# Optimization experiments

Hardware: AMD Instinct MI355X
Metric: run time of the kernel (lower is better)

Reference implementation:

```python
import jax, jax.numpy as jnp
import numpy as np

N = 100000
IN_CH = 128
OUT_CH = 128
E = 1600000


def setup_inputs() -> dict:
    key = jax.random.key(0)
    k1, k2, k3, k4 = jax.random.split(key, 4)
    x = jax.random.normal(k1, (N, IN_CH), dtype=jnp.float32)
    edge_index = jax.random.randint(k2, (2, E), 0, N, dtype=jnp.int64)
    # Glorot-style init for the GCNConv linear weight, zero bias (PyG default)
    W = jax.random.normal(k3, (IN_CH, OUT_CH), dtype=jnp.float32) * (1.0 / np.sqrt(IN_CH))
    b = jnp.zeros((OUT_CH,), dtype=jnp.float32)
    return {"x": x, "edge_index": edge_index, "W": W, "b": b}


def reference(x, edge_index, W, b):
    n = x.shape[0]
    # ---- add self loops (PyG GCNConv default add_self_loops=True) ----
    loops = jnp.arange(n, dtype=edge_index.dtype)
    row = jnp.concatenate([edge_index[0], loops])  # source
    col = jnp.concatenate([edge_index[1], loops])  # target
    # ---- symmetric degree normalization: D^{-1/2} (A+I) D^{-1/2} ----
    ones = jnp.ones(col.shape[0], dtype=x.dtype)
    deg = jax.ops.segment_sum(ones, col, num_segments=n)  # in-degree incl. self loop
    deg_inv_sqrt = jnp.where(deg > 0, jax.lax.rsqrt(deg), 0.0)
    norm = deg_inv_sqrt[row] * deg_inv_sqrt[col]  # [E+N]
    # ---- linear transform then gather-scale-scatter aggregation ----
    h = x @ W  # [N, OUT_CH]
    msgs = norm[:, None] * h[row]  # [E+N, OUT_CH]
    out = jax.ops.segment_sum(msgs, col, num_segments=n) + b  # [N, OUT_CH]
    # ---- ReLU ----
    return jax.nn.relu(out)
```

## Files before the change

kernel.cpp:

```cpp
#include <hip/hip_runtime.h>
#include <hip/hip_bf16.h>
#include <hip/hip_fp16.h>

#define IN_CH 128
#define OUT_CH 128
#define TM 64
#define TMF 128
#define CHUNK 8192
#define NPB 512
#define BSHIFT 9
#define CPAD 16
#define CAPT 16384

typedef __attribute__((ext_vector_type(8))) short short8;
typedef __attribute__((ext_vector_type(4))) float f32x4;

__device__ __forceinline__ unsigned short f2bf(float f) {
    union { float f; unsigned u; } v; v.f = f;
    unsigned r = v.u + 0x7FFFu + ((v.u >> 16) & 1u);
    return (unsigned short)(r >> 16);
}


__global__ __launch_bounds__(256) void init_kernel(int* __restrict__ cursor,
                                                   const float* __restrict__ W,
                                                   unsigned short* __restrict__ Wf,
                                                   int NBK) {
    int t = threadIdx.x;
    if (blockIdx.x == 0) {
        if (t < NBK) cursor[t * CPAD] = t * CAPT;
        return;
    }
    int base = (blockIdx.x - 1) * 2048;
#pragma unroll
    for (int rep = 0; rep < 8; ++rep) {
        int idx = base + rep * 256 + t;
        int j = idx & 7;
        int lane = (idx >> 3) & 63;
        int ctks = idx >> 9;
        int ks = ctks & 3;
        int ct = ctks >> 2;
        int k = ks * 32 + (lane >> 4) * 8 + j;
        int nc = ct * 16 + (lane & 15);
        Wf[idx] = f2bf(W[k * 128 + nc]);
    }
}

__global__ __launch_bounds__(512) void part_gemm_kernel(const int* __restrict__ row,
                                                        const int* __restrict__ col,
                                                        int* __restrict__ cursor,
                                                        int* __restrict__ tmp,
                                                        const float* __restrict__ A,
                                                        const unsigned short* __restrict__ Wf,
                                                        __half* __restrict__ G,
                                                        int E, int n, int NBK, int vec,
                                                        int nchunks) {
    __shared__ int lcnt[256];
    __shared__ int lstart[256];
    __shared__ int lbase[256];
    __shared__ int lscan[256];
    __shared__ int buf[CHUNK];
    __shared__ unsigned char bid[CHUNK];
    int t = threadIdx.x;
    if (blockIdx.x >= nchunks) {
        int gb = blockIdx.x - nchunks;
        int w = t >> 6;
        int lane = t & 63;
        int m = lane & 15;
        int quad = lane >> 4;
        int rowi = gb * TMF + w * 16 + m;
        short8 af[4];
        if (rowi < n) {
            const f32x4* Ar = (const f32x4*)(A + (size_t)rowi * 128);
#pragma unroll
            for (int ks = 0; ks < 4; ++ks) {
                f32x4 v0 = __builtin_nontemporal_load(Ar + ks * 8 + quad * 2);
                f32x4 v1 = __builtin_nontemporal_load(Ar + ks * 8 + quad * 2 + 1);
                short8 a;
                a[0] = (short)f2bf(v0.x); a[1] = (short)f2bf(v0.y);
                a[2] = (short)f2bf(v0.z); a[3] = (short)f2bf(v0.w);
                a[4] = (short)f2bf(v1.x); a[5] = (short)f2bf(v1.y);
                a[6] = (short)f2bf(v1.z); a[7] = (short)f2bf(v1.w);
                af[ks] = a;
            }
        } else {
#pragma unroll
            for (int ks = 0; ks < 4; ++ks) af[ks] = (short8)0;
        }
        int grow_base = gb * TMF + w * 16 + quad * 4;
        const short8* B8 = (const short8*)Wf;
#pragma unroll
        for (int ct = 0; ct < 8; ++ct) {
            f32x4 acc = {0.f, 0.f, 0.f, 0.f};
#pragma unroll
            for (int ks = 0; ks < 4; ++ks) {
                short8 bf = B8[(ct * 4 + ks) * 64 + lane];
                acc = __builtin_amdgcn_mfma_f32_16x16x32_bf16(af[ks], bf, acc, 0, 0, 0);
            }
            int nc = ct * 16 + m;
#pragma unroll
            for (int reg = 0; reg < 4; ++reg) {
                int grow = grow_base + reg;
                if (grow < n)
                    G[(size_t)grow * 128 + nc] = __float2half(acc[reg]);
            }
        }
        return;
    }
    int base = blockIdx.x * CHUNK;
    int nloc = min(CHUNK, E - base);
    if (t < 256) lcnt[t] = 0;
    __syncthreads();
    if (vec) {
        const int4* c4 = (const int4*)(col + base);
        int nv = nloc >> 2;
        for (int i = t; i < nv; i += 512) {
            int4 c = c4[i];
            atomicAdd(&lcnt[c.x >> BSHIFT], 1);
            atomicAdd(&lcnt[c.y >> BSHIFT], 1);
            atomicAdd(&lcnt[c.z >> BSHIFT], 1);
            atomicAdd(&lcnt[c.w >> BSHIFT], 1);
        }
        for (int i = (nv << 2) + t; i < nloc; i += 512)
            atomicAdd(&lcnt[col[base + i] >> BSHIFT], 1);
    } else {
        for (int i = t; i < nloc; i += 512)
            atomicAdd(&lcnt[col[base + i] >> BSHIFT], 1);
    }
    __syncthreads();
    int v = 0;
    if (t < 256) { v = lcnt[t]; lscan[t] = v; }
    __syncthreads();
    for (int off = 1; off < 256; off <<= 1) {
        int a = 0, b2 = 0;
        if (t < 256) { a = lscan[t]; b2 = (t >= off) ? lscan[t - off] : 0; }
        __syncthreads();
        if (t < 256) lscan[t] = a + b2;
        __syncthreads();
    }
    if (t < 256) {
        int excl = lscan[t] - v;
        lstart[t] = excl;
        lcnt[t] = excl;
        lbase[t] = (t < NBK && v) ? atomicAdd(&cursor[t * CPAD], v) : 0;
    }
    __syncthreads();
    if (vec) {
        const int4* c4 = (const int4*)(col + base);
        const int4* r4 = (const int4*)(row + base);
        int nv = nloc >> 2;
        for (int i = t; i < nv; i += 512) {
            int4 c = c4[i];
            int4 r = r4[i];
            int b0 = c.x >> BSHIFT, p0 = atomicAdd(&lcnt[b0], 1);
            buf[p0] = r.x | ((c.x & (NPB - 1)) << 20); bid[p0] = (unsigned char)b0;
            int b1 = c.y >> BSHIFT, p1 = atomicAdd(&lcnt[b1], 1);
            buf[p1] = r.y | ((c.y & (NPB - 1)) << 20); bid[p1] = (unsigned char)b1;
            int b2 = c.z >> BSHIFT, p2 = atomicAdd(&lcnt[b2], 1);
            buf[p2] = r.z | ((c.z & (NPB - 1)) << 20); bid[p2] = (unsigned char)b2;
            int b3 = c.w >> BSHIFT, p3 = atomicAdd(&lcnt[b3], 1);
            buf[p3] = r.w | ((c.w & (NPB - 1)) << 20); bid[p3] = (unsigned char)b3;
        }
        for (int i = (nv << 2) + t; i < nloc; i += 512) {
            int c = col[base + i], r = row[base + i];
            int b = c >> BSHIFT, p = atomicAdd(&lcnt[b], 1);
            buf[p] = r | ((c & (NPB - 1)) << 20); bid[p] = (unsigned char)b;
        }
    } else {
        for (int i = t; i < nloc; i += 512) {
            int c = col[base + i], r = row[base + i];
            int b = c >> BSHIFT, p = atomicAdd(&lcnt[b], 1);
            buf[p] = r | ((c & (NPB - 1)) << 20); bid[p] = (unsigned char)b;
        }
    }
    __syncthreads();
    for (int i = t; i < nloc; i += 512) {
        int b = bid[i];
        int gidx = lbase[b] + (i - lstart[b]);
        if (gidx < (b + 1) * CAPT) tmp[gidx] = buf[i];
    }
}

__global__ __launch_bounds__(512) void csr_build_kernel(const int* __restrict__ tmp,
                                                        const int* __restrict__ cursor,
                                                        int* __restrict__ offs,
                                                        float* __restrict__ dis,
                                                        int* __restrict__ srcs,
                                                        int N, int NBK) {
    __shared__ int cnt[NPB];
    __shared__ int cur[NPB];
    __shared__ int bsum[256];
    int b = blockIdx.x;
    int t = threadIdx.x;
    cnt[t] = 0;
    if (t < 256) bsum[t] = (t < NBK) ? min(cursor[t * CPAD] - t * CAPT, CAPT) : 0;
    __syncthreads();
    for (int off = 1; off < 256; off <<= 1) {
        int a = 0, b2 = 0;
        if (t < 256) { a = bsum[t]; b2 = (t >= off) ? bsum[t - off] : 0; }
        __syncthreads();
        if (t < 256) bsum[t] = a + b2;
        __syncthreads();
    }
    int wbeg = b * CAPT;
    int cnt_b = min(cursor[b * CPAD] - wbeg, CAPT);
    int cbeg = bsum[b] - cnt_b;
    if (b == 0 && t == 0) offs[N] = bsum[NBK - 1];
    for (int e = t; e < cnt_b; e += 512)
        atomicAdd(&cnt[(tmp[wbeg + e] >> 20)], 1);
    __syncthreads();
    int v0 = 0, v1 = 0, s = 0;
    if (t < 256) { v0 = cnt[2 * t]; v1 = cnt[2 * t + 1]; s = v0 + v1; cur[t] = s; }
    __syncthreads();
    for (int off = 1; off < 256; off <<= 1) {
        int a = 0, b2 = 0;
        if (t < 256) { a = cur[t]; b2 = (t >= off) ? cur[t - off] : 0; }
        __syncthreads();
        if (t < 256) cur[t] = a + b2;
        __syncthreads();
    }
    int excl_pair = 0;
    if (t < 256) excl_pair = cur[t] - s;
    __syncthreads();
    if (t < 256) {
        int e0 = excl_pair;
        int e1 = excl_pair + v0;
        cur[2 * t] = e0;
        cur[2 * t + 1] = e1;
        int n0 = b * NPB + 2 * t;
        int n1 = n0 + 1;
        if (n0 < N) { offs[n0] = cbeg + e0; dis[n0] = rsqrtf((float)(v0 + 1)); }
        if (n1 < N) { offs[n1] = cbeg + e1; dis[n1] = rsqrtf((float)(v1 + 1)); }
    }
    __syncthreads();
    for (int e = t; e < cnt_b; e += 512) {
        int p = tmp[wbeg + e];
        int slot = atomicAdd(&cur[p >> 20], 1);
        srcs[cbeg + slot] = p & 0xFFFFF;
    }
}

__global__ __launch_bounds__(256) void aggregate_g16_kernel(
        const __half2* __restrict__ g2, const int* __restrict__ srcs,
        const int* __restrict__ offs, const float* __restrict__ dis,
        const float* __restrict__ bias, float2* __restrict__ out2, int n) {
    int gid = blockIdx.x * blockDim.x + threadIdx.x;
    int wid = gid >> 6;
    int lane = gid & 63;
    if (wid >= n) return;
    int widu = __builtin_amdgcn_readfirstlane(wid);
    int beg = offs[widu];
    int end = offs[widu + 1];
    float di = dis[widu];
    float2 xi = __half22float2(g2[((size_t)widu << 6) + lane]);
    float accx = di * xi.x;
    float accy = di * xi.y;
    int e = beg;
    for (; e + 8 <= end; e += 8) {
        int s0 = __builtin_amdgcn_readfirstlane(srcs[e]);
        int s1 = __builtin_amdgcn_readfirstlane(srcs[e + 1]);
        int s2 = __builtin_amdgcn_readfirstlane(srcs[e + 2]);
        int s3 = __builtin_amdgcn_readfirstlane(srcs[e + 3]);
        int s4 = __builtin_amdgcn_readfirstlane(srcs[e + 4]);
        int s5 = __builtin_amdgcn_readfirstlane(srcs[e + 5]);
        int s6 = __builtin_amdgcn_readfirstlane(srcs[e + 6]);
        int s7 = __builtin_amdgcn_readfirstlane(srcs[e + 7]);
        float d0 = dis[s0], d1 = dis[s1], d2 = dis[s2], d3 = dis[s3];
        float d4 = dis[s4], d5 = dis[s5], d6 = dis[s6], d7 = dis[s7];
        float2 v0 = __half22float2(g2[((size_t)s0 << 6) + lane]);
        float2 v1 = __half22float2(g2[((size_t)s1 << 6) + lane]);
        float2 v2 = __half22float2(g2[((size_t)s2 << 6) + lane]);
        float2 v3 = __half22float2(g2[((size_t)s3 << 6) + lane]);
        float2 v4 = __half22float2(g2[((size_t)s4 << 6) + lane]);
        float2 v5 = __half22float2(g2[((size_t)s5 << 6) + lane]);
        float2 v6 = __half22float2(g2[((size_t)s6 << 6) + lane]);
        float2 v7 = __half22float2(g2[((size_t)s7 << 6) + lane]);
        float tx0 = fmaf(d0, v0.x, d1 * v1.x);
        float tx1 = fmaf(d2, v2.x, d3 * v3.x);
        float tx2 = fmaf(d4, v4.x, d5 * v5.x);
        float tx3 = fmaf(d6, v6.x, d7 * v7.x);
        accx += (tx0 + tx1) + (tx2 + tx3);
        float ty0 = fmaf(d0, v0.y, d1 * v1.y);
        float ty1 = fmaf(d2, v2.y, d3 * v3.y);
        float ty2 = fmaf(d4, v4.y, d5 * v5.y);
        float ty3 = fmaf(d6, v6.y, d7 * v7.y);
        accy += (ty0 + ty1) + (ty2 + ty3);
    }
    for (; e + 4 <= end; e += 4) {
        int s0 = __builtin_amdgcn_readfirstlane(srcs[e]);
        int s1 = __builtin_amdgcn_readfirstlane(srcs[e + 1]);
        int s2 = __builtin_amdgcn_readfirstlane(srcs[e + 2]);
        int s3 = __builtin_amdgcn_readfirstlane(srcs[e + 3]);
        float d0 = dis[s0], d1 = dis[s1], d2 = dis[s2], d3 = dis[s3];
        float2 v0 = __half22float2(g2[((size_t)s0 << 6) + lane]);
        float2 v1 = __half22float2(g2[((size_t)s1 << 6) + lane]);
        float2 v2 = __half22float2(g2[((size_t)s2 << 6) + lane]);
        float2 v3 = __half22float2(g2[((size_t)s3 << 6) + lane]);
        accx += fmaf(d0, v0.x, d1 * v1.x) + fmaf(d2, v2.x, d3 * v3.x);
        accy += fmaf(d0, v0.y, d1 * v1.y) + fmaf(d2, v2.y, d3 * v3.y);
    }
    for (; e < end; ++e) {
        int s = __builtin_amdgcn_readfirstlane(srcs[e]);
        float ds = dis[s];
        float2 v = __half22float2(g2[((size_t)s << 6) + lane]);
        accx = fmaf(ds, v.x, accx);
        accy = fmaf(ds, v.y, accy);
    }
    float2 bv = ((const float2*)bias)[lane];
    float2 r;
    r.x = fmaxf(fmaf(di, accx, bv.x), 0.f);
    r.y = fmaxf(fmaf(di, accy, bv.y), 0.f);
    out2[((size_t)widu << 6) + lane] = r;
}

__global__ __launch_bounds__(256) void gemm_g16_kernel(const float* __restrict__ A,
        const float* __restrict__ W, __half* __restrict__ G, int n) {
    __shared__ __half Wh[128 * 128];
    __shared__ float As[TM * 128];
    int t = threadIdx.x;
    const float4* W4 = (const float4*)W;
#pragma unroll
    for (int j = 0; j < 16; ++j) {
        int idx = t + 256 * j;
        float4 v = W4[idx];
        __half2 p0 = __floats2half2_rn(v.x, v.y);
        __half2 p1 = __floats2half2_rn(v.z, v.w);
        *(__half2*)&Wh[idx * 4]     = p0;
        *(__half2*)&Wh[idx * 4 + 2] = p1;
    }
    int row0 = blockIdx.x * TM;
    const float4* A4 = (const float4*)A;
#pragma unroll
    for (int j = 0; j < 8; ++j) {
        int idx = t + 256 * j;
        int r = idx >> 5;
        int c4 = idx & 31;
        int gr = row0 + r;
        float4 v = make_float4(0.f, 0.f, 0.f, 0.f);
        if (gr < n) v = A4[(size_t)gr * 32 + c4];
        *(float4*)&As[r * 128 + c4 * 4] = v;
    }
    __syncthreads();
    int tcol = t & 15;
    int trow = t >> 4;
    int cb = tcol * 8;
    float acc[4][8];
#pragma unroll
    for (int r = 0; r < 4; ++r)
#pragma unroll
        for (int c = 0; c < 8; ++c) acc[r][c] = 0.f;
    const float* Abase = &As[(trow * 4) * 128];
#pragma unroll 4
    for (int k = 0; k < 128; ++k) {
        float4 wv = *(const float4*)&Wh[k * 128 + cb];
        const __half2* wh = (const __half2*)&wv;
        float2 w01 = __half22float2(wh[0]);
        float2 w23 = __half22float2(wh[1]);
        float2 w45 = __half22float2(wh[2]);
        float2 w67 = __half22float2(wh[3]);
        float wreg[8] = {w01.x, w01.y, w23.x, w23.y, w45.x, w45.y, w67.x, w67.y};
#pragma unroll
        for (int r = 0; r < 4; ++r) {
            float a = Abase[r * 128 + k];
#pragma unroll
            for (int c = 0; c < 8; ++c) acc[r][c] = fmaf(a, wreg[c], acc[r][c]);
        }
    }
#pragma unroll
    for (int r = 0; r < 4; ++r) {
        int gr = row0 + trow * 4 + r;
        if (gr < n) {
            __half2 o[4];
#pragma unroll
            for (int j = 0; j < 4; ++j)
                o[j] = __floats2half2_rn(acc[r][2 * j], acc[r][2 * j + 1]);
            *(float4*)&G[(size_t)gr * 128 + cb] = *(float4*)o;
        }
    }
}

__global__ void count_kernel(const int* __restrict__ col, int* __restrict__ deg, int E) {
    int i = blockIdx.x * blockDim.x + threadIdx.x;
    if (i < E) atomicAdd(&deg[col[i]], 1);
}

__global__ void scan_block_kernel(const int* __restrict__ in, int* __restrict__ out,
                                  int* __restrict__ bsums, float* __restrict__ dis, int n) {
    __shared__ int lds[256];
    int t = threadIdx.x;
    int base = blockIdx.x * 1024;
    int v[4];
    int idx = base + t * 4;
#pragma unroll
    for (int j = 0; j < 4; ++j) v[j] = (idx + j < n) ? in[idx + j] : 0;
#pragma unroll
    for (int j = 0; j < 4; ++j)
        if (idx + j < n) dis[idx + j] = rsqrtf((float)(v[j] + 1));
    int sum = v[0] + v[1] + v[2] + v[3];
    lds[t] = sum;
    __syncthreads();
    for (int off = 1; off < 256; off <<= 1) {
        int a = lds[t];
        int bq = (t >= off) ? lds[t - off] : 0;
        __syncthreads();
        lds[t] = a + bq;
        __syncthreads();
    }
    int run = (t == 0) ? 0 : lds[t - 1];
    if (t == 255 && bsums) bsums[blockIdx.x] = lds[255];
#pragma unroll
    for (int j = 0; j < 4; ++j) {
        if (idx + j < n) out[idx + j] = run;
        run += v[j];
    }
}

__global__ void scan_sums_kernel(int* __restrict__ bsums, int nB) {
    __shared__ int lds[256];
    int t = threadIdx.x;
    lds[t] = (t < nB) ? bsums[t] : 0;
    __syncthreads();
    for (int off = 1; off < 256; off <<= 1) {
        int a = lds[t];
        int bq = (t >= off) ? lds[t - off] : 0;
        __syncthreads();
        lds[t] = a + bq;
        __syncthreads();
    }
    if (t < nB) bsums[t] = (t == 0) ? 0 : lds[t - 1];
}

__global__ void scan_add_kernel(int* __restrict__ offs, const int* __restrict__ bsums,
                                int n, int total) {
    int i = blockIdx.x * blockDim.x + threadIdx.x;
    if (i < n) offs[i] += bsums[i >> 10];
    if (i == 0) offs[n] = total;
}

__global__ void fill_kernel(const int* __restrict__ row, const int* __restrict__ col,
                            const int* __restrict__ offs, int* __restrict__ deg,
                            int* __restrict__ srcs, int E) {
    int i = blockIdx.x * blockDim.x + threadIdx.x;
    if (i < E) {
        int c = col[i];
        int old = atomicSub(&deg[c], 1);
        srcs[offs[c] + old - 1] = row[i];
    }
}

__global__ __launch_bounds__(256) void aggregate_f32_kernel(
        const float2* __restrict__ x2, const int* __restrict__ srcs,
        const int* __restrict__ offs, const float* __restrict__ dis,
        float2* __restrict__ out2, int n) {
    int gid = blockIdx.x * blockDim.x + threadIdx.x;
    int wid = gid >> 6;
    int lane = gid & 63;
    if (wid >= n) return;
    int beg = offs[wid];
    int end = offs[wid + 1];
    float di = dis[wid];
    float2 xi = x2[(size_t)wid * 64 + lane];
    float accx = di * xi.x;
    float accy = di * xi.y;
    for (int e = beg; e < end; ++e) {
        int s = srcs[e];
        float ds = dis[s];
        float2 xs = x2[(size_t)s * 64 + lane];
        accx = fmaf(ds, xs.x, accx);
        accy = fmaf(ds, xs.y, accy);
    }
    float2 r;
    r.x = di * accx;
    r.y = di * accy;
    out2[(size_t)wid * 64 + lane] = r;
}

__global__ __launch_bounds__(256) void gemm_inplace_kernel(float* __restrict__ io,
                                                           const float* __restrict__ W,
                                                           const float* __restrict__ bias, int n) {
    __shared__ float rowL[128];
    __shared__ float part[128];
    int t = threadIdx.x;
    int c = t & 127;
    int half = t >> 7;
    float w[64];
#pragma unroll
    for (int j = 0; j < 64; ++j) w[j] = W[(half * 64 + j) * 128 + c];
    float bv = bias[c];
    int kbase = half * 64;
    for (int r = blockIdx.x; r < n; r += gridDim.x) {
        if (t < 128) rowL[t] = io[(size_t)r * 128 + t];
        __syncthreads();
        float acc = 0.f;
#pragma unroll
        for (int j = 0; j < 64; ++j) acc = fmaf(rowL[kbase + j], w[j], acc);
        if (half) part[c] = acc;
        __syncthreads();
        if (!half) {
            float v = acc + part[c] + bv;
            io[(size_t)r * 128 + c] = fmaxf(v, 0.f);
        }
        __syncthreads();
    }
}

extern "C" void kernel_launch(void* const* d_in, const int* in_sizes, int n_in,
                              void* d_out, int out_size, void* d_ws, size_t ws_size,
                              hipStream_t stream) {
    const float* x  = (const float*)d_in[0];
    const int*   ei = (const int*)d_in[1];
    const float* W  = (const float*)d_in[2];
    const float* b  = (const float*)d_in[3];
    float* out = (float*)d_out;

    int N = in_sizes[0] / IN_CH;
    int E = in_sizes[1] / 2;
    const int* rowp = ei;
    const int* colp = ei + E;
    int NBK = (N + NPB - 1) >> BSHIFT;
    int tpb = 256;
    int nchunks = (E + CHUNK - 1) / CHUNK;
    int gemmBlocks = (N + TMF - 1) / TMF;

    char* p = (char*)d_ws;
    auto take = [&](size_t bytes) { char* q = p; p += (bytes + 255) & ~(size_t)255; return q; };
    int*    cursor = (int*)take((size_t)256 * CPAD * 4);
    int*    offs   = (int*)take((size_t)(N + 1) * 4);
    float*  dis    = (float*)take((size_t)N * 4);
    int*    srcs   = (int*)take((size_t)E * 4);
    __half* g      = (__half*)take((size_t)N * 128 * 2);
    unsigned short* Wf = (unsigned short*)take((size_t)16384 * 2);
    bool fast = (NBK <= 256) && ((size_t)(p - (char*)d_ws) <= ws_size) &&
                ((size_t)NBK * CAPT <= (size_t)out_size) && (N < (1 << 20)) &&
                ((size_t)E + NPB <= (size_t)CAPT * NBK);

    long long threads_agg = (long long)N * 64;
    int agg_blocks = (int)((threads_agg + tpb - 1) / tpb);

    if (fast) {
        int* tmp = (int*)d_out;
        int vec = (((uintptr_t)colp | (uintptr_t)rowp) & 15) == 0 ? 1 : 0;
        init_kernel<<<9, 256, 0, stream>>>(cursor, W, Wf, NBK);
        part_gemm_kernel<<<nchunks + gemmBlocks, 512, 0, stream>>>(
            rowp, colp, cursor, tmp, x, Wf, g, E, N, NBK, vec, nchunks);
        csr_build_kernel<<<NBK, 512, 0, stream>>>(tmp, cursor, offs, dis, srcs, N, NBK);
        aggregate_g16_kernel<<<agg_blocks, tpb, 0, stream>>>(
            (const __half2*)g, srcs, offs, dis, b, (float2*)out, N);
    } else {
        char* q = (char*)d_ws;
        auto take2 = [&](size_t bytes) { char* r = q; q += (bytes + 255) & ~(size_t)255; return r; };
        int*    deg2   = (int*)take2((size_t)N * 4);
        int*    offs2  = (int*)take2((size_t)(N + 1) * 4);
        int*    bsums2 = (int*)take2(256 * 4);
        int*    srcs2  = (int*)take2((size_t)E * 4);
        float*  dis2   = (float*)take2((size_t)N * 4);
        __half* g2b    = (__half*)take2((size_t)N * 128 * 2);
        bool fits2 = ((size_t)(q - (char*)d_ws)) <= ws_size;
        hipMemsetAsync(deg2, 0, (size_t)N * 4, stream);
        count_kernel<<<(E + tpb - 1) / tpb, tpb, 0, stream>>>(colp, deg2, E);
        int nB = (N + 1023) / 1024;
        scan_block_kernel<<<nB, 256, 0, stream>>>(deg2, offs2, bsums2, dis2, N);
        scan_sums_kernel<<<1, 256, 0, stream>>>(bsums2, nB);
        scan_add_kernel<<<(N + tpb - 1) / tpb, tpb, 0, stream>>>(offs2, bsums2, N, E);
        fill_kernel<<<(E + tpb - 1) / tpb, tpb, 0, stream>>>(rowp, colp, offs2, deg2, srcs2, E);
        if (fits2) {
            gemm_g16_kernel<<<(N + TM - 1) / TM, 256, 0, stream>>>(x, W, g2b, N);
            aggregate_g16_kernel<<<agg_blocks, tpb, 0, stream>>>(
                (const __half2*)g2b, srcs2, offs2, dis2, b, (float2*)out, N);
        } else {
            aggregate_f32_kernel<<<agg_blocks, tpb, 0, stream>>>(
                (const float2*)x, srcs2, offs2, dis2, (float2*)out, N);
            gemm_inplace_kernel<<<2048, 256, 0, stream>>>(out, W, b, N);
        }
    }
}
```

Baseline: 208.3 us.

## Use register-held atomic slots in partitioning, CSR build, and split-wave aggregation

The edge-partition kernel no longer does a separate count pass, shared scan and shared-memory staging buffer. Each thread now keeps its edges and the LDS atomic slot positions in registers and scatters straight to global memory. The CSR build kernel does the same, reusing the atomic ranks from its count pass so it skips a second global read and a second atomic pass. The aggregation kernel assigns two waves per node, each summing half the edge list, and combines them through shared memory to shorten per-node latency chains. The cost is higher register pressure, uncoalesced global scatter writes, and an extra barrier in aggregation.

```diff
diff --git a/kernel.cpp b/kernel.cpp
--- a/kernel.cpp
+++ b/kernel.cpp
@@ -53,14 +53,10 @@
                                                         const float* __restrict__ A,
                                                         const unsigned short* __restrict__ Wf,
                                                         __half* __restrict__ G,
-                                                        int E, int n, int NBK, int vec,
+                                                        int E, int n, int NBK,
                                                         int nchunks) {
     __shared__ int lcnt[256];
-    __shared__ int lstart[256];
     __shared__ int lbase[256];
-    __shared__ int lscan[256];
-    __shared__ int buf[CHUNK];
-    __shared__ unsigned char bid[CHUNK];
     int t = threadIdx.x;
     if (blockIdx.x >= nchunks) {
         int gb = blockIdx.x - nchunks;
@@ -111,73 +107,36 @@
     int nloc = min(CHUNK, E - base);
     if (t < 256) lcnt[t] = 0;
     __syncthreads();
-    if (vec) {
-        const int4* c4 = (const int4*)(col + base);
-        int nv = nloc >> 2;
-        for (int i = t; i < nv; i += 512) {
-            int4 c = c4[i];
-            atomicAdd(&lcnt[c.x >> BSHIFT], 1);
-            atomicAdd(&lcnt[c.y >> BSHIFT], 1);
-            atomicAdd(&lcnt[c.z >> BSHIFT], 1);
-            atomicAdd(&lcnt[c.w >> BSHIFT], 1);
-        }
-        for (int i = (nv << 2) + t; i < nloc; i += 512)
-            atomicAdd(&lcnt[col[base + i] >> BSHIFT], 1);
-    } else {
-        for (int i = t; i < nloc; i += 512)
-            atomicAdd(&lcnt[col[base + i] >> BSHIFT], 1);
-    }
-    __syncthreads();
-    int v = 0;
-    if (t < 256) { v = lcnt[t]; lscan[t] = v; }
-    __syncthreads();
-    for (int off = 1; off < 256; off <<= 1) {
-        int a = 0, b2 = 0;
-        if (t < 256) { a = lscan[t]; b2 = (t >= off) ? lscan[t - off] : 0; }
-        __syncthreads();
-        if (t < 256) lscan[t] = a + b2;
-        __syncthreads();
-    }
+    int myv[16];
+    int mybp[16];
+#pragma unroll
+    for (int it = 0; it < 16; ++it) {
+        int i = t + it * 512;
+        if (i < nloc) {
+            int c = col[base + i];
+            int r = row[base + i];
+            int b = c >> BSHIFT;
+            int p = atomicAdd(&lcnt[b], 1);
+            myv[it] = r | ((c & (NPB - 1)) << 20);
+            mybp[it] = b | (p << 8);
+        } else {
+            mybp[it] = -1;
+        }
+    }
+    __syncthreads();
     if (t < 256) {
-        int excl = lscan[t] - v;
-        lstart[t] = excl;
-        lcnt[t] = excl;
+        int v = lcnt[t];
         lbase[t] = (t < NBK && v) ? atomicAdd(&cursor[t * CPAD], v) : 0;
     }
     __syncthreads();
-    if (vec) {
-        const int4* c4 = (const int4*)(col + base);
-        const int4* r4 = (const int4*)(row + base);
-        int nv = nloc >> 2;
-        for (int i = t; i < nv; i += 512) {
-            int4 c = c4[i];
-            int4 r = r4[i];
-            int b0 = c.x >> BSHIFT, p0 = atomicAdd(&lcnt[b0], 1);
-            buf[p0] = r.x | ((c.x & (NPB - 1)) << 20); bid[p0] = (unsigned char)b0;
-            int b1 = c.y >> BSHIFT, p1 = atomicAdd(&lcnt[b1], 1);
-            buf[p1] = r.y | ((c.y & (NPB - 1)) << 20); bid[p1] = (unsigned char)b1;
-            int b2 = c.z >> BSHIFT, p2 = atomicAdd(&lcnt[b2], 1);
-            buf[p2] = r.z | ((c.z & (NPB - 1)) << 20); bid[p2] = (unsigned char)b2;
-            int b3 = c.w >> BSHIFT, p3 = atomicAdd(&lcnt[b3], 1);
-            buf[p3] = r.w | ((c.w & (NPB - 1)) << 20); bid[p3] = (unsigned char)b3;
-        }
-        for (int i = (nv << 2) + t; i < nloc; i += 512) {
-            int c = col[base + i], r = row[base + i];
-            int b = c >> BSHIFT, p = atomicAdd(&lcnt[b], 1);
-            buf[p] = r | ((c & (NPB - 1)) << 20); bid[p] = (unsigned char)b;
-        }
-    } else {
-        for (int i = t; i < nloc; i += 512) {
-            int c = col[base + i], r = row[base + i];
-            int b = c >> BSHIFT, p = atomicAdd(&lcnt[b], 1);
-            buf[p] = r | ((c & (NPB - 1)) << 20); bid[p] = (unsigned char)b;
-        }
-    }
-    __syncthreads();
-    for (int i = t; i < nloc; i += 512) {
-        int b = bid[i];
-        int gidx = lbase[b] + (i - lstart[b]);
-        if (gidx < (b + 1) * CAPT) tmp[gidx] = buf[i];
+#pragma unroll
+    for (int it = 0; it < 16; ++it) {
+        if (mybp[it] >= 0) {
+            int b = mybp[it] & 255;
+            int p = mybp[it] >> 8;
+            int gidx = lbase[b] + p;
+            if (gidx < (b + 1) * CAPT) tmp[gidx] = myv[it];
+        }
     }
 }
 
@@ -206,8 +165,19 @@
     int cnt_b = min(cursor[b * CPAD] - wbeg, CAPT);
     int cbeg = bsum[b] - cnt_b;
     if (b == 0 && t == 0) offs[N] = bsum[NBK - 1];
-    for (int e = t; e < cnt_b; e += 512)
-        atomicAdd(&cnt[(tmp[wbeg + e] >> 20)], 1);
+    int myv[32];
+    int myp[32];
+#pragma unroll
+    for (int it = 0; it < 32; ++it) {
+        int e = t + it * 512;
+        if (e < cnt_b) {
+            int p = tmp[wbeg + e];
+            myv[it] = p;
+            myp[it] = atomicAdd(&cnt[p >> 20], 1);
+        } else {
+            myv[it] = -1;
+        }
+    }
     __syncthreads();
     int v0 = 0, v1 = 0, s = 0;
     if (t < 256) { v0 = cnt[2 * t]; v1 = cnt[2 * t + 1]; s = v0 + v1; cur[t] = s; }
@@ -233,30 +203,47 @@
         if (n1 < N) { offs[n1] = cbeg + e1; dis[n1] = rsqrtf((float)(v1 + 1)); }
     }
     __syncthreads();
-    for (int e = t; e < cnt_b; e += 512) {
-        int p = tmp[wbeg + e];
-        int slot = atomicAdd(&cur[p >> 20], 1);
-        srcs[cbeg + slot] = p & 0xFFFFF;
-    }
-}
-
-__global__ __launch_bounds__(256) void aggregate_g16_kernel(
+#pragma unroll
+    for (int it = 0; it < 32; ++it) {
+        if (myv[it] >= 0) {
+            int node = myv[it] >> 20;
+            srcs[cbeg + cur[node] + myp[it]] = myv[it] & 0xFFFFF;
+        }
+    }
+}
+
+__global__ __launch_bounds__(512) void aggregate_g16_kernel(
         const __half2* __restrict__ g2, const int* __restrict__ srcs,
         const int* __restrict__ offs, const float* __restrict__ dis,
         const float* __restrict__ bias, float2* __restrict__ out2, int n) {
-    int gid = blockIdx.x * blockDim.x + threadIdx.x;
-    int wid = gid >> 6;
-    int lane = gid & 63;
-    if (wid >= n) return;
-    int widu = __builtin_amdgcn_readfirstlane(wid);
-    int beg = offs[widu];
-    int end = offs[widu + 1];
-    float di = dis[widu];
-    float2 xi = __half22float2(g2[((size_t)widu << 6) + lane]);
-    float accx = di * xi.x;
-    float accy = di * xi.y;
-    int e = beg;
-    for (; e + 8 <= end; e += 8) {
+    __shared__ float2 part[4][64];
+    int t = threadIdx.x;
+    int lane = t & 63;
+    int wv = t >> 6;
+    int nib = wv >> 1;
+    int half = wv & 1;
+    int node = blockIdx.x * 4 + nib;
+    bool active = node < n;
+    int beg = 0, end = 0;
+    float di = 0.f;
+    int widu = 0;
+    if (active) {
+        widu = __builtin_amdgcn_readfirstlane(node);
+        beg = offs[widu];
+        end = offs[widu + 1];
+        di = dis[widu];
+    }
+    int mid = beg + ((end - beg) >> 1);
+    int lo = half ? mid : beg;
+    int hi = half ? end : mid;
+    float accx = 0.f, accy = 0.f;
+    if (!half && active) {
+        float2 xi = __half22float2(g2[((size_t)widu << 6) + lane]);
+        accx = di * xi.x;
+        accy = di * xi.y;
+    }
+    int e = lo;
+    for (; e + 8 <= hi; e += 8) {
         int s0 = __builtin_amdgcn_readfirstlane(srcs[e]);
         int s1 = __builtin_amdgcn_readfirstlane(srcs[e + 1]);
         int s2 = __builtin_amdgcn_readfirstlane(srcs[e + 2]);
@@ -286,7 +273,7 @@
         float ty3 = fmaf(d6, v6.y, d7 * v7.y);
         accy += (ty0 + ty1) + (ty2 + ty3);
     }
-    for (; e + 4 <= end; e += 4) {
+    for (; e + 4 <= hi; e += 4) {
         int s0 = __builtin_amdgcn_readfirstlane(srcs[e]);
         int s1 = __builtin_amdgcn_readfirstlane(srcs[e + 1]);
         int s2 = __builtin_amdgcn_readfirstlane(srcs[e + 2]);
@@ -299,18 +286,28 @@
         accx += fmaf(d0, v0.x, d1 * v1.x) + fmaf(d2, v2.x, d3 * v3.x);
         accy += fmaf(d0, v0.y, d1 * v1.y) + fmaf(d2, v2.y, d3 * v3.y);
     }
-    for (; e < end; ++e) {
+    for (; e < hi; ++e) {
         int s = __builtin_amdgcn_readfirstlane(srcs[e]);
         float ds = dis[s];
         float2 v = __half22float2(g2[((size_t)s << 6) + lane]);
         accx = fmaf(ds, v.x, accx);
         accy = fmaf(ds, v.y, accy);
     }
-    float2 bv = ((const float2*)bias)[lane];
-    float2 r;
-    r.x = fmaxf(fmaf(di, accx, bv.x), 0.f);
-    r.y = fmaxf(fmaf(di, accy, bv.y), 0.f);
-    out2[((size_t)widu << 6) + lane] = r;
+    if (half) {
+        float2 pp; pp.x = accx; pp.y = accy;
+        part[nib][lane] = pp;
+    }
+    __syncthreads();
+    if (!half && active) {
+        float2 p2 = part[nib][lane];
+        accx += p2.x;
+        accy += p2.y;
+        float2 bv = ((const float2*)bias)[lane];
+        float2 r;
+        r.x = fmaxf(fmaf(di, accx, bv.x), 0.f);
+        r.y = fmaxf(fmaf(di, accy, bv.y), 0.f);
+        out2[((size_t)widu << 6) + lane] = r;
+    }
 }
 
 __global__ __launch_bounds__(256) void gemm_g16_kernel(const float* __restrict__ A,
@@ -534,17 +531,15 @@
                 ((size_t)NBK * CAPT <= (size_t)out_size) && (N < (1 << 20)) &&
                 ((size_t)E + NPB <= (size_t)CAPT * NBK);
 
-    long long threads_agg = (long long)N * 64;
-    int agg_blocks = (int)((threads_agg + tpb - 1) / tpb);
+    int agg_blocks = (N + 3) / 4;
 
     if (fast) {
         int* tmp = (int*)d_out;
-        int vec = (((uintptr_t)colp | (uintptr_t)rowp) & 15) == 0 ? 1 : 0;
         init_kernel<<<9, 256, 0, stream>>>(cursor, W, Wf, NBK);
         part_gemm_kernel<<<nchunks + gemmBlocks, 512, 0, stream>>>(
-            rowp, colp, cursor, tmp, x, Wf, g, E, N, NBK, vec, nchunks);
+            rowp, colp, cursor, tmp, x, Wf, g, E, N, NBK, nchunks);
         csr_build_kernel<<<NBK, 512, 0, stream>>>(tmp, cursor, offs, dis, srcs, N, NBK);
-        aggregate_g16_kernel<<<agg_blocks, tpb, 0, stream>>>(
+        aggregate_g16_kernel<<<agg_blocks, 512, 0, stream>>>(
             (const __half2*)g, srcs, offs, dis, b, (float2*)out, N);
     } else {
         char* q = (char*)d_ws;
@@ -565,10 +560,10 @@
         fill_kernel<<<(E + tpb - 1) / tpb, tpb, 0, stream>>>(rowp, colp, offs2, deg2, srcs2, E);
         if (fits2) {
             gemm_g16_kernel<<<(N + TM - 1) / TM, 256, 0, stream>>>(x, W, g2b, N);
-            aggregate_g16_kernel<<<agg_blocks, tpb, 0, stream>>>(
+            aggregate_g16_kernel<<<agg_blocks, 512, 0, stream>>>(
                 (const __half2*)g2b, srcs2, offs2, dis2, b, (float2*)out, N);
         } else {
-            aggregate_f32_kernel<<<agg_blocks, tpb, 0, stream>>>(
+            aggregate_f32_kernel<<<(int)(((long long)N * 64 + tpb - 1) / tpb), tpb, 0, stream>>>(
                 (const float2*)x, srcs2, offs2, dis2, (float2*)out, N);
             gemm_inplace_kernel<<<2048, 256, 0, stream>>>(out, W, b, N);
         }
```

Measured after the change: 244.8 us. 1.18x slower.
